# Performance work log

Hardware: AMD Instinct MI355X
Metric: run time of the kernel (lower is better)

The kernel has to match this reference:

```python
import jax, jax.numpy as jnp
import numpy as np

N_ITER = 15
ITER_LR = 0.1


def setup_inputs() -> dict:
    key = jax.random.key(0)
    ks = jax.random.split(key, 4)
    dims = [784, 512, 256, 10]
    x = jax.random.normal(ks[0], (32768, dims[0]), dtype=jnp.float32)
    # weights[i]: (dims[i+1], dims[i]) scaled by sqrt(2/dims[i+1]); biases[i]: (dims[i],) zeros
    W0 = jax.random.normal(ks[1], (dims[1], dims[0]), dtype=jnp.float32) * np.sqrt(2.0 / dims[1]).astype(np.float32)
    W1 = jax.random.normal(ks[2], (dims[2], dims[1]), dtype=jnp.float32) * np.sqrt(2.0 / dims[2]).astype(np.float32)
    W2 = jax.random.normal(ks[3], (dims[3], dims[2]), dtype=jnp.float32) * np.sqrt(2.0 / dims[3]).astype(np.float32)
    b0 = jnp.zeros((dims[0],), dtype=jnp.float32)
    b1 = jnp.zeros((dims[1],), dtype=jnp.float32)
    b2 = jnp.zeros((dims[2],), dtype=jnp.float32)
    return {"x": x, "W0": W0, "W1": W1, "W2": W2, "b0": b0, "b1": b1, "b2": b2}


def reference(x, W0, W1, W2, b0, b1, b2):
    # feedforward pass: mus[i+1] = relu(mus[i] @ W[i].T)
    m1 = jax.nn.relu(x @ W0.T)    # [B, 512]
    m2 = jax.nn.relu(m1 @ W1.T)   # [B, 256]
    m3 = jax.nn.relu(m2 @ W2.T)   # [B, 10]

    # iterative predictive-coding updates: for l in {1, 2}:
    #   pred = relu(mus[l+1] @ W[l] + b[l]); mus[l] = relu(mus[l] - iter_lr * (mus[l] - pred))
    def body(_, carry):
        m1, m2, m3 = carry
        pred1 = jax.nn.relu(m2 @ W1 + b1)                 # uses m2 before its update (loop order)
        m1 = jax.nn.relu(m1 - ITER_LR * (m1 - pred1))
        pred2 = jax.nn.relu(m3 @ W2 + b2)
        m2 = jax.nn.relu(m2 - ITER_LR * (m2 - pred2))
        return (m1, m2, m3)

    m1, m2, m3 = jax.lax.fori_loop(0, N_ITER, body, (m1, m2, m3))
    # mus[-1] is never updated by the loop; returned as-is (faithful to the torch code)
    return m3
```

## Files before the change

kernel.cpp:

```cpp
#include <hip/hip_runtime.h>

typedef __bf16 bhalf;
typedef bhalf bhalf8 __attribute__((ext_vector_type(8)));
typedef float f32x4 __attribute__((ext_vector_type(4)));
typedef unsigned short u16;
typedef u16 u16x8 __attribute__((ext_vector_type(8)));

__device__ __forceinline__ u16 f2bf(float f) {
  union { float f; unsigned u; } v; v.f = f;
  unsigned r = v.u + 0x7FFFu + ((v.u >> 16) & 1u);
  return (u16)(r >> 16);
}

__device__ __forceinline__ int swz(int L) { return L ^ (((L >> 7) & 7) << 4); }

#define GLL16(gp, lp) __builtin_amdgcn_global_load_lds( \
    (const __attribute__((address_space(1))) unsigned int*)(gp), \
    (__attribute__((address_space(3))) unsigned int*)(lp), 16, 0, 0)

#define SB() __builtin_amdgcn_sched_barrier(0)

#define KP0 832
#define W0E (512 * KP0)
#define W1E (256 * 512)
#define W2E (16 * 256)

__global__ __launch_bounds__(256) void cvt_weights(
    const float* __restrict__ W0, const float* __restrict__ W1,
    const float* __restrict__ W2,
    u16* __restrict__ W0b, u16* __restrict__ W1b, u16* __restrict__ W2b)
{
  int i = blockIdx.x * 256 + threadIdx.x;
  if (i < W0E) {
    int r = i / KP0, k = i - r * KP0;
    W0b[i] = (k < 784) ? f2bf(W0[r * 784 + k]) : (u16)0;
    return;
  }
  i -= W0E;
  if (i < W1E) { W1b[i] = f2bf(W1[i]); return; }
  i -= W1E;
  if (i < W2E) {
    int r = i >> 8, c = i & 255;
    W2b[i] = (r < 10) ? f2bf(W2[r * 256 + c]) : (u16)0;
  }
}

__global__ __launch_bounds__(512) void gemm1_p8(
    const float* __restrict__ x, const u16* __restrict__ Wb, u16* __restrict__ Cp)
{
  extern __shared__ u16 ldsu[];
  char* lds = (char*)ldsu;
  const int t = threadIdx.x, w = t >> 6, lane = t & 63;
  const size_t rbase = (size_t)blockIdx.x * 128;
  const int wr = w >> 2, wc = w & 3, fr = lane & 15, fg = lane >> 4;

  int aO[4];
#pragma unroll
  for (int m = 0; m < 4; ++m) aO[m] = swz((wr * 64 + m * 16 + fr) * 128 + fg * 16);
  int bO[4];
#pragma unroll
  for (int j = 0; j < 4; ++j) bO[j] = swz((wc * 128 + j * 16 + fr) * 64 + fg * 16);

  const u16* bSrcP[4];
#pragma unroll
  for (int i = 0; i < 4; ++i) {
    int P = (w * 4 + i) * 1024 + lane * 16;
    int U = swz(P);
    bSrcP[i] = Wb + (size_t)(U >> 6) * KP0 + ((U & 63) >> 1);
  }
  const float* xRow[2]; int aKc[2];
#pragma unroll
  for (int c2 = 0; c2 < 2; ++c2) {
    int P = c2 * 8192 + t * 16;
    int U = swz(P);
    xRow[c2] = x + (rbase + (U >> 7)) * (size_t)784;
    aKc[c2] = (U & 127) >> 1;
  }

  f32x4 acc[4][8];
#pragma unroll
  for (int m = 0; m < 4; ++m)
#pragma unroll
    for (int n = 0; n < 8; ++n) acc[m][n] = (f32x4){0.f, 0.f, 0.f, 0.f};

  bhalf8 afA[4], bf[4];
  f32x4 xrE[2][2], xrO[2][2];

  auto loadX = [&](int tt2, f32x4 (&xr)[2][2]) {
#pragma unroll
    for (int c2 = 0; c2 < 2; ++c2) {
      int k = tt2 * 64 + aKc[c2];
      const float* p = xRow[c2] + ((k < 784) ? k : 0);
      xr[c2][0] = *(const f32x4*)p; xr[c2][1] = *(const f32x4*)(p + 4);
    }
  };
  auto cvtW = [&](int aB, f32x4 (&xr)[2][2]) {
#pragma unroll
    for (int c2 = 0; c2 < 2; ++c2) {
      u16x8 v;
#pragma unroll
      for (int j = 0; j < 4; ++j) { v[j] = f2bf(xr[c2][0][j]); v[4 + j] = f2bf(xr[c2][1][j]); }
      *(u16x8*)(lds + aB + c2 * 8192 + t * 16) = v;
    }
  };
  auto gllLo = [&](int H) {
    char* bb = lds + 32768 + (H % 3) * 32768;
    GLL16(bSrcP[0] + H * 32, bb + (w * 4 + 0) * 1024);
    GLL16(bSrcP[1] + H * 32, bb + (w * 4 + 1) * 1024);
  };
  auto gllHi = [&](int H) {
    char* bb = lds + 32768 + (H % 3) * 32768;
    GLL16(bSrcP[2] + H * 32, bb + (w * 4 + 2) * 1024);
    GLL16(bSrcP[3] + H * 32, bb + (w * 4 + 3) * 1024);
  };
  auto rdA = [&](int aB, int ks) {
#pragma unroll
    for (int m = 0; m < 4; ++m)
      afA[m] = *(const bhalf8*)(lds + aB + (aO[m] ^ (ks << 6)));
  };
  auto rdBq = [&](int H, int hi) {
    const char* bb = lds + 32768 + (H % 3) * 32768 + hi * 4096;
#pragma unroll
    for (int j = 0; j < 4; ++j) bf[j] = *(const bhalf8*)(bb + bO[j]);
  };
  auto mfmaLoQ = [&]() {
    __builtin_amdgcn_s_setprio(1);
#pragma unroll
    for (int m = 0; m < 4; ++m)
#pragma unroll
      for (int n = 0; n < 4; ++n)
        acc[m][n] = __builtin_amdgcn_mfma_f32_16x16x32_bf16(afA[m], bf[n], acc[m][n], 0, 0, 0);
    __builtin_amdgcn_s_setprio(0);
  };
  auto mfmaHiQ = [&]() {
    __builtin_amdgcn_s_setprio(1);
#pragma unroll
    for (int m = 0; m < 4; ++m)
#pragma unroll
      for (int n = 0; n < 4; ++n)
        acc[m][4 + n] = __builtin_amdgcn_mfma_f32_16x16x32_bf16(afA[m], bf[n], acc[m][4 + n], 0, 0, 0);
    __builtin_amdgcn_s_setprio(0);
  };

  auto tile = [&](int tt, f32x4 (&xrLd)[2][2], f32x4 (&xrCv)[2][2],
                  bool doStage, bool doX, int vmPh4, bool vm0Ph2) {
    const int aB = (tt & 1) * 16384;
    const int H0 = 2 * tt, H1 = 2 * tt + 1;
    rdA(aB, 0); rdBq(H0, 0);
    if (doStage) gllLo(H0 + 2);
    __builtin_amdgcn_s_barrier();
    asm volatile("s_waitcnt lgkmcnt(0)" ::: "memory"); SB();
    mfmaLoQ();
    __builtin_amdgcn_s_barrier();
    rdBq(H0, 1);
    if (doStage) gllHi(H0 + 2);
    __builtin_amdgcn_s_barrier();
    asm volatile("s_waitcnt lgkmcnt(0)" ::: "memory"); SB();
    mfmaHiQ();
    if (vm0Ph2) { asm volatile("s_waitcnt vmcnt(0)" ::: "memory"); }
    else        { asm volatile("s_waitcnt vmcnt(4)" ::: "memory"); }
    __builtin_amdgcn_s_barrier();
    rdA(aB, 1); rdBq(H1, 0);
    if (doStage) gllLo(H1 + 2);
    if (doX) loadX(tt + 2, xrLd);
    __builtin_amdgcn_s_barrier();
    asm volatile("s_waitcnt lgkmcnt(0)" ::: "memory"); SB();
    mfmaLoQ();
    __builtin_amdgcn_s_barrier();
    rdBq(H1, 1);
    if (tt < 12) cvtW(aB ^ 16384, xrCv);
    if (doStage) gllHi(H1 + 2);
    __builtin_amdgcn_s_barrier();
    asm volatile("s_waitcnt lgkmcnt(0)" ::: "memory"); SB();
    mfmaHiQ();
    if (vmPh4 == 8)      { asm volatile("s_waitcnt vmcnt(8)" ::: "memory"); }
    else if (vmPh4 == 4) { asm volatile("s_waitcnt vmcnt(4)" ::: "memory"); }
    __builtin_amdgcn_s_barrier();
  };

  gllLo(0); gllHi(0);
  gllLo(1); gllHi(1);
  loadX(0, xrE);
  loadX(1, xrO);
  cvtW(0, xrE);
  asm volatile("s_waitcnt lgkmcnt(0)" ::: "memory");
  __builtin_amdgcn_s_barrier();

  for (int i = 0; i < 5; ++i) {
    tile(2 * i,     xrE, xrO, true, true, 8, false);
    tile(2 * i + 1, xrO, xrE, true, true, 8, false);
  }
  tile(10, xrE, xrO, true,  true,  8, false);
  tile(11, xrO, xrE, true,  false, 4, false);
  tile(12, xrE, xrO, false, false, -1, true);

#pragma unroll
  for (int m = 0; m < 4; ++m)
#pragma unroll
    for (int n = 0; n < 8; ++n)
#pragma unroll
      for (int q = 0; q < 4; ++q) {
        size_t row = rbase + wr * 64 + m * 16 + fg * 4 + q;
        size_t col = (size_t)wc * 128 + n * 16 + fr;
        float vv = acc[m][n][q];
        vv = vv > 0.f ? vv : 0.f;
        Cp[row * 512 + col] = f2bf(vv);
      }
}

__global__ __launch_bounds__(512, 4) void gemm23(
    const u16* __restrict__ m1, const u16* __restrict__ W1b,
    const u16* __restrict__ W2b, float* __restrict__ out)
{
  __shared__ u16 pool[20480];
  __shared__ u16 W2s[16][264];
  const int t = threadIdx.x, w = t >> 6, lane = t & 63;
  const size_t rbase = (size_t)blockIdx.x * 64;
  const int wr = w >> 2, wc = w & 3, fr = lane & 15, fg = lane >> 4;

  {
    int r = t >> 5, kc = (t & 31) * 8;
    *(int4*)&W2s[r][kc] = *(const int4*)(W2b + r * 256 + kc);
  }

  int aOff[2], bOff[4];
#pragma unroll
  for (int i = 0; i < 2; ++i) aOff[i] = swz((wr * 32 + i * 16 + fr) * 64 + fg * 16);
#pragma unroll
  for (int j = 0; j < 4; ++j) bOff[j] = swz((wc * 64 + j * 16 + fr) * 64 + fg * 16);

  const u16* aSrc = nullptr; int aDst = 0;
  if (w < 4) {
    int Dl = (w * 64 + lane) * 16;
    int Ul = swz(Dl);
    aSrc = m1 + (rbase + (Ul >> 6)) * 512 + ((Ul & 63) >> 1);
    aDst = (w * 64) * 16;
  }
  const u16* bSrc[2]; int bDst[2];
#pragma unroll
  for (int i = 0; i < 2; ++i) {
    int Dl = (w * 128 + i * 64 + lane) * 16;
    int Ul = swz(Dl);
    bSrc[i] = W1b + (Ul >> 6) * 512 + ((Ul & 63) >> 1);
    bDst[i] = 8192 + (w * 128 + i * 64) * 16;
  }

  f32x4 acc[2][4];
#pragma unroll
  for (int i = 0; i < 2; ++i)
#pragma unroll
    for (int j = 0; j < 4; ++j) acc[i][j] = (f32x4){0.f, 0.f, 0.f, 0.f};

  if (w < 4) GLL16(aSrc, (char*)pool + aDst);
#pragma unroll
  for (int i = 0; i < 2; ++i) GLL16(bSrc[i], (char*)pool + bDst[i]);

  for (int tt = 0; tt < 16; ++tt) {
    const int cur = tt & 1;
    const char* Asc = (const char*)pool + cur * 4096;
    const char* Bsc = (const char*)pool + 8192 + cur * 16384;
    asm volatile("s_waitcnt vmcnt(0)" ::: "memory");
    __syncthreads();

    if (tt < 15) {
      const int k0 = (tt + 1) * 32;
      if (w < 4) GLL16(aSrc + k0, (char*)pool + (cur ^ 1) * 4096 + aDst);
#pragma unroll
      for (int i = 0; i < 2; ++i)
        GLL16(bSrc[i] + k0, (char*)pool + (cur ^ 1) * 16384 + bDst[i]);
    }

    bhalf8 af[2], bfv[4];
#pragma unroll
    for (int i = 0; i < 2; ++i) af[i] = *(const bhalf8*)(Asc + aOff[i]);
#pragma unroll
    for (int j = 0; j < 4; ++j) bfv[j] = *(const bhalf8*)(Bsc + bOff[j]);
#pragma unroll
    for (int i = 0; i < 2; ++i)
#pragma unroll
      for (int j = 0; j < 4; ++j)
        acc[i][j] = __builtin_amdgcn_mfma_f32_16x16x32_bf16(af[i], bfv[j], acc[i][j], 0, 0, 0);
  }

  __syncthreads();
#pragma unroll
  for (int i = 0; i < 2; ++i)
#pragma unroll
    for (int j = 0; j < 4; ++j)
#pragma unroll
      for (int q = 0; q < 4; ++q) {
        int row = wr * 32 + i * 16 + fg * 4 + q;
        int col = wc * 64 + j * 16 + fr;
        float vv = acc[i][j][q];
        vv = vv > 0.f ? vv : 0.f;
        pool[row * 264 + col] = f2bf(vv);
      }
  __syncthreads();

  if (w < 4) {
    f32x4 acc3 = (f32x4){0.f, 0.f, 0.f, 0.f};
    const int arow = w * 16 + fr;
#pragma unroll
    for (int ks = 0; ks < 8; ++ks) {
      bhalf8 a = *(const bhalf8*)&pool[arow * 264 + ks * 32 + fg * 8];
      bhalf8 b = *(const bhalf8*)&W2s[fr][ks * 32 + fg * 8];
      acc3 = __builtin_amdgcn_mfma_f32_16x16x32_bf16(a, b, acc3, 0, 0, 0);
    }
    if (fr < 10) {
#pragma unroll
      for (int q = 0; q < 4; ++q) {
        size_t row = rbase + w * 16 + fg * 4 + q;
        float vv = acc3[q];
        out[row * 10 + fr] = vv > 0.f ? vv : 0.f;
      }
    }
  }
}

extern "C" void kernel_launch(void* const* d_in, const int* in_sizes, int n_in,
                              void* d_out, int out_size, void* d_ws, size_t ws_size,
                              hipStream_t stream) {
  const float* x  = (const float*)d_in[0];
  const float* W0 = (const float*)d_in[1];
  const float* W1 = (const float*)d_in[2];
  const float* W2 = (const float*)d_in[3];
  float* out = (float*)d_out;

  char* ws = (char*)d_ws;
  u16* m1  = (u16*)(ws);
  u16* W0b = (u16*)(ws + 33554432);
  u16* W1b = (u16*)(ws + 34406400);
  u16* W2b = (u16*)(ws + 34668544);

  hipFuncSetAttribute((const void*)gemm1_p8,
                      hipFuncAttributeMaxDynamicSharedMemorySize, 131072);

  cvt_weights<<<dim3((W0E + W1E + W2E + 255) / 256), dim3(256), 0, stream>>>(
      W0, W1, W2, W0b, W1b, W2b);

  gemm1_p8<<<dim3(256), dim3(512), 131072, stream>>>(x, W0b, m1);

  gemm23<<<dim3(512), dim3(512), 0, stream>>>(m1, W1b, W2b, out);
}
```

Before: 62.76 us.

## Fuse layer-2 and layer-3 GEMMs into the first GEMM kernel via LDS

Merges the separate gemm23 kernel into the first GEMM kernel. The ReLU'd m1 tile stays in LDS in two 64-row halves and feeds the W1 GEMM (W1 streamed with double-buffered global-to-LDS loads), then the small W2 GEMM, which writes the output directly. This removes the 32 MB bf16 m1 round trip through global memory and one kernel launch. In exchange each block does the second-stage work serially after the first GEMM with only 256 blocks, so there is less parallelism and less latency hiding for that stage, and W1 is reloaded by every block.

```diff
diff --git a/kernel.cpp b/kernel.cpp
--- a/kernel.cpp
+++ b/kernel.cpp
@@ -12,7 +12,8 @@
   return (u16)(r >> 16);
 }
 
-__device__ __forceinline__ int swz(int L) { return L ^ (((L >> 7) & 7) << 4); }
+__device__ __forceinline__ int swz(int L)  { return L ^ (((L >> 7)  & 7) << 4); }
+__device__ __forceinline__ int swz2(int L) { return L ^ (((L >> 10) & 7) << 4); }
 
 #define GLL16(gp, lp) __builtin_amdgcn_global_load_lds( \
     (const __attribute__((address_space(1))) unsigned int*)(gp), \
@@ -45,8 +46,10 @@
   }
 }
 
-__global__ __launch_bounds__(512) void gemm1_p8(
-    const float* __restrict__ x, const u16* __restrict__ Wb, u16* __restrict__ Cp)
+__global__ __launch_bounds__(512) void fused3(
+    const float* __restrict__ x, const u16* __restrict__ Wb,
+    const u16* __restrict__ W1b, const u16* __restrict__ W2b,
+    float* __restrict__ out)
 {
   extern __shared__ u16 ldsu[];
   char* lds = (char*)ldsu;
@@ -194,126 +197,115 @@
   tile(11, xrO, xrE, true,  false, 4, false);
   tile(12, xrE, xrO, false, false, -1, true);
 
-#pragma unroll
-  for (int m = 0; m < 4; ++m)
-#pragma unroll
-    for (int n = 0; n < 8; ++n)
-#pragma unroll
-      for (int q = 0; q < 4; ++q) {
-        size_t row = rbase + wr * 64 + m * 16 + fg * 4 + q;
-        size_t col = (size_t)wc * 128 + n * 16 + fr;
-        float vv = acc[m][n][q];
-        vv = vv > 0.f ? vv : 0.f;
-        Cp[row * 512 + col] = f2bf(vv);
+  const int wr2 = w >> 2, wc2 = w & 3;
+  const u16* w1Src[4];
+#pragma unroll
+  for (int i = 0; i < 4; ++i) {
+    int P = (w * 4 + i) * 1024 + lane * 16;
+    int U = swz(P);
+    w1Src[i] = W1b + (size_t)(U >> 7) * 512 + ((U & 127) >> 1);
+  }
+  int a2O[2];
+#pragma unroll
+  for (int m = 0; m < 2; ++m) a2O[m] = (wr2 * 32 + m * 16 + fr) * 1024 + fg * 16;
+  int b2O[4];
+#pragma unroll
+  for (int n = 0; n < 4; ++n) b2O[n] = (wc2 * 64 + n * 16 + fr) * 128 + fg * 16;
+
+  for (int h = 0; h < 2; ++h) {
+    if (wr == h) {
+#pragma unroll
+      for (int m = 0; m < 4; ++m)
+#pragma unroll
+        for (int n = 0; n < 8; ++n)
+#pragma unroll
+          for (int q = 0; q < 4; ++q) {
+            int row = m * 16 + fg * 4 + q;
+            int col = wc * 128 + n * 16 + fr;
+            float vv = acc[m][n][q];
+            vv = vv > 0.f ? vv : 0.f;
+            *(u16*)(lds + swz2(row * 1024 + col * 2)) = f2bf(vv);
+          }
+    }
+    __syncthreads();
+
+    f32x4 acc2[2][4];
+#pragma unroll
+    for (int m = 0; m < 2; ++m)
+#pragma unroll
+      for (int n = 0; n < 4; ++n) acc2[m][n] = (f32x4){0.f, 0.f, 0.f, 0.f};
+
+#pragma unroll
+    for (int i = 0; i < 4; ++i) GLL16(w1Src[i], lds + 65536 + (w * 4 + i) * 1024);
+
+    for (int kt = 0; kt < 8; ++kt) {
+      const char* wb = lds + 65536 + (kt & 1) * 32768;
+      asm volatile("s_waitcnt vmcnt(0)" ::: "memory");
+      __syncthreads();
+      if (kt < 7) {
+#pragma unroll
+        for (int i = 0; i < 4; ++i)
+          GLL16(w1Src[i] + (kt + 1) * 64, lds + 65536 + ((kt + 1) & 1) * 32768 + (w * 4 + i) * 1024);
       }
-}
-
-__global__ __launch_bounds__(512, 4) void gemm23(
-    const u16* __restrict__ m1, const u16* __restrict__ W1b,
-    const u16* __restrict__ W2b, float* __restrict__ out)
-{
-  __shared__ u16 pool[20480];
-  __shared__ u16 W2s[16][264];
-  const int t = threadIdx.x, w = t >> 6, lane = t & 63;
-  const size_t rbase = (size_t)blockIdx.x * 64;
-  const int wr = w >> 2, wc = w & 3, fr = lane & 15, fg = lane >> 4;
-
-  {
-    int r = t >> 5, kc = (t & 31) * 8;
-    *(int4*)&W2s[r][kc] = *(const int4*)(W2b + r * 256 + kc);
-  }
-
-  int aOff[2], bOff[4];
-#pragma unroll
-  for (int i = 0; i < 2; ++i) aOff[i] = swz((wr * 32 + i * 16 + fr) * 64 + fg * 16);
-#pragma unroll
-  for (int j = 0; j < 4; ++j) bOff[j] = swz((wc * 64 + j * 16 + fr) * 64 + fg * 16);
-
-  const u16* aSrc = nullptr; int aDst = 0;
-  if (w < 4) {
-    int Dl = (w * 64 + lane) * 16;
-    int Ul = swz(Dl);
-    aSrc = m1 + (rbase + (Ul >> 6)) * 512 + ((Ul & 63) >> 1);
-    aDst = (w * 64) * 16;
-  }
-  const u16* bSrc[2]; int bDst[2];
-#pragma unroll
-  for (int i = 0; i < 2; ++i) {
-    int Dl = (w * 128 + i * 64 + lane) * 16;
-    int Ul = swz(Dl);
-    bSrc[i] = W1b + (Ul >> 6) * 512 + ((Ul & 63) >> 1);
-    bDst[i] = 8192 + (w * 128 + i * 64) * 16;
-  }
-
-  f32x4 acc[2][4];
-#pragma unroll
-  for (int i = 0; i < 2; ++i)
-#pragma unroll
-    for (int j = 0; j < 4; ++j) acc[i][j] = (f32x4){0.f, 0.f, 0.f, 0.f};
-
-  if (w < 4) GLL16(aSrc, (char*)pool + aDst);
-#pragma unroll
-  for (int i = 0; i < 2; ++i) GLL16(bSrc[i], (char*)pool + bDst[i]);
-
-  for (int tt = 0; tt < 16; ++tt) {
-    const int cur = tt & 1;
-    const char* Asc = (const char*)pool + cur * 4096;
-    const char* Bsc = (const char*)pool + 8192 + cur * 16384;
-    asm volatile("s_waitcnt vmcnt(0)" ::: "memory");
+#pragma unroll
+      for (int ks = 0; ks < 2; ++ks) {
+        bhalf8 a2[2], b2[4];
+#pragma unroll
+        for (int m = 0; m < 2; ++m)
+          a2[m] = *(const bhalf8*)(lds + swz2(a2O[m] + kt * 128 + ks * 64));
+#pragma unroll
+        for (int n = 0; n < 4; ++n)
+          b2[n] = *(const bhalf8*)(wb + swz(b2O[n] + ks * 64));
+        __builtin_amdgcn_s_setprio(1);
+#pragma unroll
+        for (int m = 0; m < 2; ++m)
+#pragma unroll
+          for (int n = 0; n < 4; ++n)
+            acc2[m][n] = __builtin_amdgcn_mfma_f32_16x16x32_bf16(a2[m], b2[n], acc2[m][n], 0, 0, 0);
+        __builtin_amdgcn_s_setprio(0);
+      }
+    }
     __syncthreads();
 
-    if (tt < 15) {
-      const int k0 = (tt + 1) * 32;
-      if (w < 4) GLL16(aSrc + k0, (char*)pool + (cur ^ 1) * 4096 + aDst);
-#pragma unroll
-      for (int i = 0; i < 2; ++i)
-        GLL16(bSrc[i] + k0, (char*)pool + (cur ^ 1) * 16384 + bDst[i]);
-    }
-
-    bhalf8 af[2], bfv[4];
-#pragma unroll
-    for (int i = 0; i < 2; ++i) af[i] = *(const bhalf8*)(Asc + aOff[i]);
-#pragma unroll
-    for (int j = 0; j < 4; ++j) bfv[j] = *(const bhalf8*)(Bsc + bOff[j]);
-#pragma unroll
-    for (int i = 0; i < 2; ++i)
-#pragma unroll
-      for (int j = 0; j < 4; ++j)
-        acc[i][j] = __builtin_amdgcn_mfma_f32_16x16x32_bf16(af[i], bfv[j], acc[i][j], 0, 0, 0);
-  }
-
-  __syncthreads();
-#pragma unroll
-  for (int i = 0; i < 2; ++i)
-#pragma unroll
-    for (int j = 0; j < 4; ++j)
-#pragma unroll
-      for (int q = 0; q < 4; ++q) {
-        int row = wr * 32 + i * 16 + fg * 4 + q;
-        int col = wc * 64 + j * 16 + fr;
-        float vv = acc[i][j][q];
-        vv = vv > 0.f ? vv : 0.f;
-        pool[row * 264 + col] = f2bf(vv);
+    u16* m2s = (u16*)(lds + 65536);
+    u16* W2s = (u16*)(lds + 99328);
+    {
+      int r = t >> 5, kc = (t & 31) * 8;
+      *(int4*)&W2s[r * 264 + kc] = *(const int4*)(W2b + r * 256 + kc);
+    }
+#pragma unroll
+    for (int m = 0; m < 2; ++m)
+#pragma unroll
+      for (int n = 0; n < 4; ++n)
+#pragma unroll
+        for (int q = 0; q < 4; ++q) {
+          int row = wr2 * 32 + m * 16 + fg * 4 + q;
+          int col = wc2 * 64 + n * 16 + fr;
+          float vv = acc2[m][n][q];
+          vv = vv > 0.f ? vv : 0.f;
+          m2s[row * 264 + col] = f2bf(vv);
+        }
+    __syncthreads();
+
+    if (w < 4) {
+      f32x4 acc3 = (f32x4){0.f, 0.f, 0.f, 0.f};
+      const int arow = w * 16 + fr;
+#pragma unroll
+      for (int ks = 0; ks < 8; ++ks) {
+        bhalf8 a = *(const bhalf8*)&m2s[arow * 264 + ks * 32 + fg * 8];
+        bhalf8 b = *(const bhalf8*)&W2s[fr * 264 + ks * 32 + fg * 8];
+        acc3 = __builtin_amdgcn_mfma_f32_16x16x32_bf16(a, b, acc3, 0, 0, 0);
       }
-  __syncthreads();
-
-  if (w < 4) {
-    f32x4 acc3 = (f32x4){0.f, 0.f, 0.f, 0.f};
-    const int arow = w * 16 + fr;
-#pragma unroll
-    for (int ks = 0; ks < 8; ++ks) {
-      bhalf8 a = *(const bhalf8*)&pool[arow * 264 + ks * 32 + fg * 8];
-      bhalf8 b = *(const bhalf8*)&W2s[fr][ks * 32 + fg * 8];
-      acc3 = __builtin_amdgcn_mfma_f32_16x16x32_bf16(a, b, acc3, 0, 0, 0);
-    }
-    if (fr < 10) {
-#pragma unroll
-      for (int q = 0; q < 4; ++q) {
-        size_t row = rbase + w * 16 + fg * 4 + q;
-        float vv = acc3[q];
-        out[row * 10 + fr] = vv > 0.f ? vv : 0.f;
+      if (fr < 10) {
+#pragma unroll
+        for (int q = 0; q < 4; ++q) {
+          size_t row = rbase + h * 64 + w * 16 + fg * 4 + q;
+          float vv = acc3[q];
+          out[row * 10 + fr] = vv > 0.f ? vv : 0.f;
+        }
       }
     }
+    __syncthreads();
   }
 }
 
@@ -327,18 +319,15 @@
   float* out = (float*)d_out;
 
   char* ws = (char*)d_ws;
-  u16* m1  = (u16*)(ws);
-  u16* W0b = (u16*)(ws + 33554432);
-  u16* W1b = (u16*)(ws + 34406400);
-  u16* W2b = (u16*)(ws + 34668544);
-
-  hipFuncSetAttribute((const void*)gemm1_p8,
+  u16* W0b = (u16*)(ws);
+  u16* W1b = (u16*)(ws + 851968);
+  u16* W2b = (u16*)(ws + 1114112);
+
+  hipFuncSetAttribute((const void*)fused3,
                       hipFuncAttributeMaxDynamicSharedMemorySize, 131072);
 
   cvt_weights<<<dim3((W0E + W1E + W2E + 255) / 256), dim3(256), 0, stream>>>(
       W0, W1, W2, W0b, W1b, W2b);
 
-  gemm1_p8<<<dim3(256), dim3(512), 131072, stream>>>(x, W0b, m1);
-
-  gemm23<<<dim3(512), dim3(512), 0, stream>>>(m1, W1b, W2b, out);
+  fused3<<<dim3(256), dim3(512), 131072, stream>>>(x, W0b, W1b, W2b, out);
 }
```

Result: slower. 140.1 us (+123.2%).
